# Kernel tuning notes

Measured on AMD Instinct MI355X. Metric: run time of the kernel, lower is better.

Reference implementation:

```python
import jax, jax.numpy as jnp
import numpy as np

B, M, L, HID, H, LAYERS = 16, 128, 512, 256, 4, 2
DH = HID // H  # 64 = head dim, also kernel_param dim


def _ln(x, g, b, eps=1e-5):
    mu = jnp.mean(x, axis=-1, keepdims=True)
    var = jnp.mean((x - mu) ** 2, axis=-1, keepdims=True)
    return (x - mu) / jnp.sqrt(var + eps) * g + b


def setup_inputs() -> dict:
    key = jax.random.key(0)
    ks = jax.random.split(key, 24)
    s = 0.05
    return {
        "ct_t": jax.random.uniform(ks[0], (B, M), jnp.float32),
        "ts_t": jax.random.uniform(ks[1], (B, L), jnp.float32),
        "ct_emb": jax.random.normal(ks[2], (B, M, HID), jnp.float32),
        "ts_emb": jax.random.normal(ks[3], (B, L, HID), jnp.float32),
        "kernel_param": jax.random.normal(ks[4], (DH,), jnp.float32),
        "ct_W": jax.random.normal(ks[5], (HID, HID), jnp.float32) * s,
        "ct_b": jnp.zeros((HID,), jnp.float32),
        "fW0": jax.random.normal(ks[6], (HID, HID), jnp.float32) * s,
        "fb0": jnp.zeros((HID,), jnp.float32),
        "fW1": jax.random.normal(ks[7], (HID, HID), jnp.float32) * s,
        "fb1": jnp.zeros((HID,), jnp.float32),
        "fW2": jax.random.normal(ks[8], (HID, HID), jnp.float32) * s,
        "fb2": jnp.zeros((HID,), jnp.float32),
        "f_ln_g": jnp.ones((HID,), jnp.float32),
        "f_ln_b": jnp.zeros((HID,), jnp.float32),
        "Wqkv": jax.random.normal(ks[9], (LAYERS, 3 * HID, HID), jnp.float32) * s,
        "bqkv": jnp.zeros((LAYERS, 3 * HID), jnp.float32),
        "Wo": jax.random.normal(ks[10], (LAYERS, HID, HID), jnp.float32) * s,
        "bo": jnp.zeros((LAYERS, HID), jnp.float32),
        "W1": jax.random.normal(ks[11], (LAYERS, 2 * HID, HID), jnp.float32) * s,
        "b1": jnp.zeros((LAYERS, 2 * HID), jnp.float32),
        "W2": jax.random.normal(ks[12], (LAYERS, HID, 2 * HID), jnp.float32) * s,
        "b2": jnp.zeros((LAYERS, HID), jnp.float32),
        "ln1_g": jnp.ones((LAYERS, HID), jnp.float32),
        "ln1_b": jnp.zeros((LAYERS, HID), jnp.float32),
        "ln2_g": jnp.ones((LAYERS, HID), jnp.float32),
        "ln2_b": jnp.zeros((LAYERS, HID), jnp.float32),
        "pred_W": jax.random.normal(ks[13], (1, HID), jnp.float32) * s,
        "pred_b": jnp.zeros((1,), jnp.float32),
    }


def reference(ct_t, ts_t, ct_emb, ts_emb, kernel_param, ct_W, ct_b,
              fW0, fb0, fW1, fb1, fW2, fb2, f_ln_g, f_ln_b,
              Wqkv, bqkv, Wo, bo, W1, b1, W2, b2,
              ln1_g, ln1_b, ln2_g, ln2_b, pred_W, pred_b):
    # --- TN tokenizer: multi-scale RBF kernel temporal fusion ---
    alpha = jax.nn.softplus(kernel_param)                       # [DH]  log(1+exp(p))
    ct_e = (jnp.einsum('bmd,ed->bme', ct_emb, ct_W) + ct_b)     # [B,M,HID]
    ct_e = ct_e.reshape(B, M, H, DH)
    diff = ct_t[:, :, None] - ts_t[:, None, :]                  # [B,M,L]
    norm = (diff * diff)[..., None]                             # [B,M,L,1]
    outs = []
    for s in range(H):                                          # fixed small loop over scales
        z = (-float(s)) * alpha * norm                          # [B,M,L,DH]
        w = jax.nn.logsumexp(z, axis=3, keepdims=True)          # [B,M,L,1]
        sim = jnp.exp(z - w)                                    # normalized kernel sims
        outs.append(jnp.einsum('bmnd,bmd->bnd', sim, ct_e[:, :, s, :]))  # scatter over ts events
    temp = jnp.concatenate(outs, axis=-1)                       # [B,L,HID]
    # --- Fusion module ---
    aux = jax.nn.elu(temp @ fW0.T + fb0 + ts_emb @ fW1.T + fb1)
    x = _ln(aux @ fW2.T + fb2 + ts_emb, f_ln_g, f_ln_b)         # [B,L,HID]
    # --- Transformer encoder (post-LN, gelu, no dropout at eval) ---
    inv_sqrt = 1.0 / np.sqrt(DH).astype(np.float32)
    for l in range(LAYERS):
        qkv = x @ Wqkv[l].T + bqkv[l]                           # [B,L,3*HID]
        q, k, v = jnp.split(qkv, 3, axis=-1)
        def heads(t):
            return t.reshape(B, L, H, DH).transpose(0, 2, 1, 3)
        q, k, v = heads(q), heads(k), heads(v)
        att = jax.nn.softmax(jnp.einsum('bhqd,bhkd->bhqk', q, k) * inv_sqrt, axis=-1)
        o = jnp.einsum('bhqk,bhkd->bhqd', att, v).transpose(0, 2, 1, 3).reshape(B, L, HID)
        x = _ln(x + o @ Wo[l].T + bo[l], ln1_g[l], ln1_b[l])
        ff = jax.nn.gelu(x @ W1[l].T + b1[l], approximate=False) @ W2[l].T + b2[l]
        x = _ln(x + ff, ln2_g[l], ln2_b[l])
    return x @ pred_W.T + pred_b                                # [B,L,1]
```

## Files before the change

kernel.cpp:

```cpp
#include <hip/hip_runtime.h>
#include <hip/hip_bf16.h>
#include <cstddef>

#define Bsz 16
#define Msz 128
#define Lsz 512
#define HIDs 256

typedef __attribute__((ext_vector_type(4))) float f32x4;
typedef __attribute__((ext_vector_type(8))) __bf16 bf16x8;
typedef __attribute__((ext_vector_type(8))) unsigned short ushort8;

#define CHEB_K 12
#define PI_F 3.14159265358979323846f

static __device__ inline unsigned short f2bf(float f) {
    __hip_bfloat16 h = __float2bfloat16(f);
    return *(unsigned short*)&h;
}
static __device__ inline float bf2f(unsigned short u) {
    return __builtin_bit_cast(float, (unsigned)u << 16);
}
static __device__ inline void gload16(const ushort* g, ushort* l) {
    __builtin_amdgcn_global_load_lds(
        (const __attribute__((address_space(1))) void*)g,
        (__attribute__((address_space(3))) void*)l, 16, 0, 0);
}

__global__ __launch_bounds__(256) void cheb_kernel(
    const float* __restrict__ kp, float* __restrict__ clut, float* __restrict__ cD)
{
    __shared__ float costab[CHEB_K][32];
    __shared__ float xq[32];
    __shared__ float alph[64];
    const int t = threadIdx.x;
    if (t < 64) {
        float p = kp[t];
        alph[t] = fmaxf(p, 0.f) + log1pf(__expf(-fabsf(p)));
    }
    #pragma unroll
    for (int i = 0; i < 2; i++) {
        int idx = i * 256 + t;
        if (idx < CHEB_K * 32) {
            int k = idx >> 5, q = idx & 31;
            float th = (q + 0.5f) * (PI_F / 32.f);
            costab[k][q] = __cosf((float)k * th);
        }
    }
    if (t < 32) xq[t] = 0.5f * (1.f + __cosf((t + 0.5f) * (PI_F / 32.f)));
    __syncthreads();

    if (t >= 192) return;
    const int d = t & 63, s1 = t >> 6;
    const float u = (float)(s1 + 1) * alph[d];
    float f[32];
    #pragma unroll
    for (int q = 0; q < 32; q++) f[q] = __expf(-u * xq[q]);
    #pragma unroll
    for (int k = 0; k < CHEB_K; k++) {
        float sum = 0.f;
        #pragma unroll
        for (int q = 0; q < 32; q++) sum = fmaf(f[q], costab[k][q], sum);
        float c = sum * ((k == 0 ? 1.f : 2.f) / 32.f);
        clut[s1 * (CHEB_K * 64) + k * 64 + d] = c;
        float sr = c;
        #pragma unroll
        for (int o = 1; o <= 32; o <<= 1) sr += __shfl_xor(sr, o, 64);
        if (d == 0) cD[s1 * CHEB_K + k] = sr;
    }
}

__global__ __launch_bounds__(256) void prep_kernel(
    const float* __restrict__ ts_emb, const float* __restrict__ ct_emb,
    const float* __restrict__ ct_W, const float* __restrict__ fW0,
    const float* __restrict__ fW1, const float* __restrict__ fW2,
    const float* __restrict__ Wqkv, const float* __restrict__ Wo,
    const float* __restrict__ W1, const float* __restrict__ W2,
    ushort* __restrict__ Xcat, ushort* __restrict__ Wcat,
    ushort* __restrict__ cebin, ushort* __restrict__ wct,
    ushort* __restrict__ wf2, ushort* __restrict__ wqkv,
    ushort* __restrict__ wo, ushort* __restrict__ w1, ushort* __restrict__ w2,
    const float* __restrict__ ct_t, const float* __restrict__ ts_t,
    const float* __restrict__ cD, ushort* __restrict__ invW)
{
    const int bid = blockIdx.x;
    const int tid = threadIdx.x;

    if (bid < 1920) {
        const unsigned u = bid * 256u + tid;
        const float* src; ushort* dst; unsigned rel;
        if (u < 262144u) {
            rel = u; src = ts_emb;
            dst = Xcat + ((size_t)(rel >> 5) * 512 + 256 + (rel & 31) * 8);
        } else if (u < 327680u) { rel = u - 262144u; src = ct_emb; dst = cebin + (size_t)rel * 8; }
        else if (u < 335872u) { rel = u - 327680u; src = ct_W; dst = wct + (size_t)rel * 8; }
        else if (u < 344064u) { rel = u - 335872u; src = fW0;
            dst = Wcat + ((size_t)(rel >> 5) * 512 + (rel & 31) * 8); }
        else if (u < 352256u) { rel = u - 344064u; src = fW1;
            dst = Wcat + ((size_t)(rel >> 5) * 512 + 256 + (rel & 31) * 8); }
        else if (u < 360448u) { rel = u - 352256u; src = fW2; dst = wf2 + (size_t)rel * 8; }
        else if (u < 409600u) { rel = u - 360448u; src = Wqkv; dst = wqkv + (size_t)rel * 8; }
        else if (u < 425984u) { rel = u - 409600u; src = Wo;  dst = wo + (size_t)rel * 8; }
        else if (u < 458752u) { rel = u - 425984u; src = W1;  dst = w1 + (size_t)rel * 8; }
        else                  { rel = u - 458752u; src = W2;  dst = w2 + (size_t)rel * 8; }
        float4 a = ((const float4*)src)[(size_t)rel * 2];
        float4 b = ((const float4*)src)[(size_t)rel * 2 + 1];
        ushort8 o;
        o[0] = f2bf(a.x); o[1] = f2bf(a.y); o[2] = f2bf(a.z); o[3] = f2bf(a.w);
        o[4] = f2bf(b.x); o[5] = f2bf(b.y); o[6] = f2bf(b.z); o[7] = f2bf(b.w);
        *(ushort8*)dst = o;
    } else {
        __shared__ float cd[3][CHEB_K];
        if (tid < 3 * CHEB_K) cd[tid / CHEB_K][tid % CHEB_K] = cD[tid];
        __syncthreads();

        const unsigned G = (bid - 1920) * 256u + tid;
        const int b = G >> 16;
        const int n = (G >> 7) & 511;
        const int m = G & 127;

        float x = ct_t[b * Msz + m] - ts_t[b * Lsz + n];
        x = x * x;
        const float xi = 2.f * x - 1.f;
        const float xi2 = 2.f * xi;

        float t0 = 1.f, t1 = xi;
        float a1 = cd[0][0] + cd[0][1] * xi;
        float a2 = cd[1][0] + cd[1][1] * xi;
        float a3 = cd[2][0] + cd[2][1] * xi;
        #pragma unroll
        for (int k = 2; k < CHEB_K; k++) {
            float tn = fmaf(xi2, t1, -t0);
            a1 = fmaf(cd[0][k], tn, a1);
            a2 = fmaf(cd[1][k], tn, a2);
            a3 = fmaf(cd[2][k], tn, a3);
            t0 = t1; t1 = tn;
        }
        const size_t base = ((size_t)b * 3 * Lsz + n) * Msz + m;
        invW[base]                         = f2bf(1.f / a1);
        invW[base + (size_t)Lsz * Msz]     = f2bf(1.f / a2);
        invW[base + (size_t)2 * Lsz * Msz] = f2bf(1.f / a3);
    }
}

__global__ __launch_bounds__(256) void gemm_mfma_kernel(
    const ushort* __restrict__ X, const ushort* __restrict__ W,
    const float* __restrict__ bias, const float* __restrict__ bias2,
    float* __restrict__ Yf, ushort* __restrict__ Yb,
    int NR, int K, int OUT, int act)
{
    __shared__ ushort As[2][64 * 64];
    __shared__ ushort Bs[2][128 * 64];

    const int nbx = OUT >> 7;
    const int bx = blockIdx.x % nbx;
    const int by = blockIdx.x / nbx;
    const int r0 = by << 6, o0 = bx << 7;
    const int tid = threadIdx.x;
    const int w = tid >> 6;
    const int lane = tid & 63;
    const int wr = w >> 1, wc = w & 1;
    const int lr = lane & 15, lg = lane >> 4;

    const int grow = lane >> 3;
    const int gchunk = (lane & 7) ^ grow;

    unsigned aoff[2][2], boff[4][2];
    #pragma unroll
    for (int f = 0; f < 2; f++) {
        unsigned cc = (unsigned)((lg + 4 * f) ^ (lr & 7)) * 16u;
        #pragma unroll
        for (int m = 0; m < 2; m++)
            aoff[m][f] = (unsigned)(wr * 32 + m * 16 + lr) * 128u + cc;
        #pragma unroll
        for (int n = 0; n < 4; n++)
            boff[n][f] = (unsigned)(wc * 64 + n * 16 + lr) * 128u + cc;
    }

    f32x4 acc[2][4];
    #pragma unroll
    for (int m = 0; m < 2; m++)
        #pragma unroll
        for (int n = 0; n < 4; n++) acc[m][n] = (f32x4){0.f, 0.f, 0.f, 0.f};

    const int nk = K >> 6;

    auto stage = [&](int buf, int ks) {
        const int k0 = ks << 6;
        #pragma unroll
        for (int i = 0; i < 2; i++) {
            int row = w * 16 + i * 8 + grow;
            gload16(X + (size_t)(r0 + row) * K + k0 + gchunk * 8,
                    &As[buf][(w * 16 + i * 8) * 64]);
        }
        #pragma unroll
        for (int i = 0; i < 4; i++) {
            int row = w * 32 + i * 8 + grow;
            gload16(W + (size_t)(o0 + row) * K + k0 + gchunk * 8,
                    &Bs[buf][(w * 32 + i * 8) * 64]);
        }
    };

    stage(0, 0);
    __syncthreads();
    int cur = 0;
    for (int ks = 0; ks < nk; ks++) {
        if (ks + 1 < nk) stage(cur ^ 1, ks + 1);
        const char* Ab = (const char*)As[cur];
        const char* Bb = (const char*)Bs[cur];
        #pragma unroll
        for (int f = 0; f < 2; f++) {
            bf16x8 av[2], bv[4];
            #pragma unroll
            for (int m = 0; m < 2; m++)
                av[m] = *(const bf16x8*)(Ab + aoff[m][f]);
            #pragma unroll
            for (int n = 0; n < 4; n++)
                bv[n] = *(const bf16x8*)(Bb + boff[n][f]);
            #pragma unroll
            for (int m = 0; m < 2; m++)
                #pragma unroll
                for (int n = 0; n < 4; n++)
                    acc[m][n] = __builtin_amdgcn_mfma_f32_16x16x32_bf16(
                        av[m], bv[n], acc[m][n], 0, 0, 0);
        }
        __syncthreads();
        cur ^= 1;
    }

    const int ocol0 = o0 + wc * 64;
    float bn[4];
    #pragma unroll
    for (int n = 0; n < 4; n++) {
        int o = ocol0 + n * 16 + lr;
        bn[n] = bias[o] + (bias2 ? bias2[o] : 0.f);
    }

    #pragma unroll
    for (int m = 0; m < 2; m++) {
        #pragma unroll
        for (int p = 0; p < 4; p++) {
            int r = r0 + wr * 32 + m * 16 + 4 * lg + p;
            size_t rb = (size_t)r * OUT;
            #pragma unroll
            for (int n = 0; n < 4; n++) {
                int o = ocol0 + n * 16 + lr;
                float v = acc[m][n][p] + bn[n];
                if (act == 1)      v = (v > 0.f) ? v : (__expf(v) - 1.f);
                else if (act == 2) v = 0.5f * v * (1.f + erff(v * 0.70710678118654752f));
                if (Yf) Yf[rb + o] = v;
                if (Yb) Yb[rb + o] = f2bf(v);
            }
        }
    }
}

__global__ __launch_bounds__(256) void gemm_ln_kernel(
    const ushort* __restrict__ X, const ushort* __restrict__ W,
    const float* __restrict__ bias, const float* __restrict__ add,
    const float* __restrict__ lng, const float* __restrict__ lnb,
    float* __restrict__ Xf, ushort* __restrict__ Xb,
    const float* __restrict__ predW, const float* __restrict__ predb,
    float* __restrict__ pout, int K)
{
    __shared__ ushort As[2][16 * 64];
    __shared__ ushort Bs[2][256 * 64];
    __shared__ float redA[16][4];
    __shared__ float redB[16][4];

    const int r0 = blockIdx.x << 4;
    const int tid = threadIdx.x;
    const int w = tid >> 6;
    const int lane = tid & 63;
    const int lr = lane & 15, lg = lane >> 4;
    const int grow = lane >> 3;
    const int gchunk = (lane & 7) ^ grow;

    unsigned aoff[2], boff[4][2];
    #pragma unroll
    for (int f = 0; f < 2; f++) {
        unsigned cc = (unsigned)((lg + 4 * f) ^ (lr & 7)) * 16u;
        aoff[f] = (unsigned)lr * 128u + cc;
        #pragma unroll
        for (int n = 0; n < 4; n++)
            boff[n][f] = (unsigned)(w * 64 + n * 16 + lr) * 128u + cc;
    }

    f32x4 acc[4];
    #pragma unroll
    for (int n = 0; n < 4; n++) acc[n] = (f32x4){0.f, 0.f, 0.f, 0.f};

    const int nk = K >> 6;

    auto stage = [&](int buf, int ks) {
        const int k0 = ks << 6;
        if (w < 2)
            gload16(X + (size_t)(r0 + w * 8 + grow) * K + k0 + gchunk * 8,
                    &As[buf][(w * 8) * 64]);
        #pragma unroll
        for (int i = 0; i < 8; i++) {
            gload16(W + (size_t)(w * 64 + i * 8 + grow) * K + k0 + gchunk * 8,
                    &Bs[buf][(w * 64 + i * 8) * 64]);
        }
    };

    stage(0, 0);
    __syncthreads();
    int cur = 0;
    for (int ks = 0; ks < nk; ks++) {
        if (ks + 1 < nk) stage(cur ^ 1, ks + 1);
        const char* Ab = (const char*)As[cur];
        const char* Bb = (const char*)Bs[cur];
        #pragma unroll
        for (int f = 0; f < 2; f++) {
            bf16x8 av = *(const bf16x8*)(Ab + aoff[f]);
            #pragma unroll
            for (int n = 0; n < 4; n++) {
                bf16x8 bv = *(const bf16x8*)(Bb + boff[n][f]);
                acc[n] = __builtin_amdgcn_mfma_f32_16x16x32_bf16(
                    av, bv, acc[n], 0, 0, 0);
            }
        }
        __syncthreads();
        cur ^= 1;
    }

    const int col0 = w * 64;
    float bn[4], gv[4], bv2[4], pwv[4];
    #pragma unroll
    for (int n = 0; n < 4; n++) {
        int o = col0 + n * 16 + lr;
        bn[n] = bias[o];
        gv[n] = lng[o];
        bv2[n] = lnb[o];
        pwv[n] = predW ? predW[o] : 0.f;
    }
    #pragma unroll
    for (int p = 0; p < 4; p++) {
        int r = r0 + 4 * lg + p;
        size_t rb = (size_t)r * 256;
        #pragma unroll
        for (int n = 0; n < 4; n++)
            acc[n][p] += bn[n] + add[rb + col0 + n * 16 + lr];
    }

    #pragma unroll
    for (int p = 0; p < 4; p++) {
        float s = acc[0][p] + acc[1][p] + acc[2][p] + acc[3][p];
        #pragma unroll
        for (int o = 1; o <= 8; o <<= 1) s += __shfl_xor(s, o);
        if (lr == 0) redA[4 * lg + p][w] = s;
    }
    __syncthreads();
    float mu[4];
    #pragma unroll
    for (int p = 0; p < 4; p++) {
        int row = 4 * lg + p;
        mu[p] = (redA[row][0] + redA[row][1] + redA[row][2] + redA[row][3])
                * (1.f / 256.f);
    }

    #pragma unroll
    for (int p = 0; p < 4; p++) {
        float q = 0.f;
        #pragma unroll
        for (int n = 0; n < 4; n++) {
            float dl = acc[n][p] - mu[p];
            q = fmaf(dl, dl, q);
        }
        #pragma unroll
        for (int o = 1; o <= 8; o <<= 1) q += __shfl_xor(q, o);
        if (lr == 0) redB[4 * lg + p][w] = q;
    }
    __syncthreads();

    #pragma unroll
    for (int p = 0; p < 4; p++) {
        int row = 4 * lg + p;
        float var = (redB[row][0] + redB[row][1] + redB[row][2] + redB[row][3])
                    * (1.f / 256.f);
        float rsig = rsqrtf(var + 1e-5f);
        int r = r0 + row;
        size_t rb = (size_t)r * 256;
        float pd = 0.f;
        #pragma unroll
        for (int n = 0; n < 4; n++) {
            int o = col0 + n * 16 + lr;
            float xn = (acc[n][p] - mu[p]) * rsig * gv[n] + bv2[n];
            if (Xf) Xf[rb + o] = xn;
            if (Xb) Xb[rb + o] = f2bf(xn);
            pd = fmaf(xn, pwv[n], pd);
        }
        if (predW) {
            #pragma unroll
            for (int o = 1; o <= 8; o <<= 1) pd += __shfl_xor(pd, o);
            if (lr == 0) redA[row][w] = pd;
        }
    }
    if (predW) {
        __syncthreads();
        if (tid < 16)
            pout[r0 + tid] = redA[tid][0] + redA[tid][1] + redA[tid][2]
                           + redA[tid][3] + predb[0];
    }
}

__global__ __launch_bounds__(256) void tokmix_kernel(
    const float* __restrict__ ct_t, const float* __restrict__ ts_t,
    const ushort* __restrict__ ceb, const ushort* __restrict__ invW,
    const float* __restrict__ clut, ushort* __restrict__ Xcat)
{
    const int bid = blockIdx.x;
    const int tid = threadIdx.x;

    if (bid < 384) {
        const int nt = bid & 7;
        const int s1 = (bid >> 3) % 3;
        const int b  = bid / 24;
        const int w = tid >> 6, lane = tid & 63, g = lane >> 4, r = lane & 15;

        __shared__ ushort ceT[64][136];
        __shared__ float  cl[CHEB_K][64];
        __shared__ float  cts[128];

        #pragma unroll
        for (int i = 0; i < 8; i++) {
            int idx = i * 256 + tid;
            int m = idx >> 4, d4 = (idx & 15) << 2;
            const ushort* gp = ceb + (((size_t)b * 128 + m) << 8) + (s1 + 1) * 64 + d4;
            ushort4 v = *(const ushort4*)gp;
            ceT[d4 + 0][m] = v.x; ceT[d4 + 1][m] = v.y;
            ceT[d4 + 2][m] = v.z; ceT[d4 + 3][m] = v.w;
        }
        #pragma unroll
        for (int i = 0; i < 3; i++) {
            int idx = i * 256 + tid;
            cl[idx >> 6][idx & 63] = clut[s1 * (CHEB_K * 64) + idx];
        }
        if (tid < 128) cts[tid] = ct_t[b * 128 + tid];
        __syncthreads();

        const int nrow = nt * 64 + w * 16 + r;
        const float tsn = ts_t[b * 512 + nrow];

        float xi2v[4][8], Ta[4][8], Tb[4][8];
        #pragma unroll
        for (int t4 = 0; t4 < 4; t4++) {
            int m0 = 8 * g + 32 * t4;
            ushort8 iv = *(const ushort8*)&invW[((((size_t)b * 3 + s1) * 512 + nrow) << 7) + m0];
            #pragma unroll
            for (int j = 0; j < 8; j++) {
                float dfx = cts[m0 + j] - tsn;
                float x = dfx * dfx;
                float xi = 2.f * x - 1.f;
                float w0 = bf2f(iv[j]);
                xi2v[t4][j] = 2.f * xi;
                Ta[t4][j] = w0;
                Tb[t4][j] = w0 * xi;
            }
        }

        bf16x8 cef[4][4];
        #pragma unroll
        for (int db = 0; db < 4; db++)
            #pragma unroll
            for (int t4 = 0; t4 < 4; t4++)
                cef[db][t4] = *(const bf16x8*)&ceT[db * 16 + r][8 * g + 32 * t4];

        f32x4 acc[4];
        #pragma unroll
        for (int db = 0; db < 4; db++) acc[db] = (f32x4){0.f, 0.f, 0.f, 0.f};

        #pragma unroll
        for (int k = 0; k < CHEB_K; k++) {
            if (k >= 2) {
                #pragma unroll
                for (int t4 = 0; t4 < 4; t4++)
                    #pragma unroll
                    for (int j = 0; j < 8; j++) {
                        if (k & 1) Tb[t4][j] = fmaf(xi2v[t4][j], Ta[t4][j], -Tb[t4][j]);
                        else       Ta[t4][j] = fmaf(xi2v[t4][j], Tb[t4][j], -Ta[t4][j]);
                    }
            }
            bf16x8 af[4];
            #pragma unroll
            for (int t4 = 0; t4 < 4; t4++) {
                ushort8 u;
                #pragma unroll
                for (int j = 0; j < 8; j++)
                    u[j] = f2bf((k & 1) ? Tb[t4][j] : Ta[t4][j]);
                af[t4] = __builtin_bit_cast(bf16x8, u);
            }
            #pragma unroll
            for (int db = 0; db < 4; db++) {
                f32x4 gk = (f32x4){0.f, 0.f, 0.f, 0.f};
                #pragma unroll
                for (int t4 = 0; t4 < 4; t4++)
                    gk = __builtin_amdgcn_mfma_f32_16x16x32_bf16(af[t4], cef[db][t4], gk, 0, 0, 0);
                float ck = cl[k][db * 16 + r];
                #pragma unroll
                for (int p = 0; p < 4; p++) acc[db][p] = fmaf(ck, gk[p], acc[db][p]);
            }
        }

        #pragma unroll
        for (int db = 0; db < 4; db++)
            #pragma unroll
            for (int p = 0; p < 4; p++) {
                int n_out = nt * 64 + w * 16 + 4 * g + p;
                Xcat[((size_t)b * 512 + n_out) * 512 + (s1 + 1) * 64 + db * 16 + r] =
                    f2bf(acc[db][p]);
            }
    } else {
        const int b = bid - 384;
        const int d = tid & 63, q = tid >> 6;
        float s = 0.f;
        #pragma unroll 8
        for (int i = 0; i < 32; i++) {
            int m = q * 32 + i;
            s += bf2f(ceb[(((size_t)b * 128 + m) << 8) + d]);
        }
        __shared__ float red0[4][64];
        __shared__ ushort row0[64];
        red0[q][d] = s;
        __syncthreads();
        if (tid < 64)
            row0[tid] = f2bf((red0[0][tid] + red0[1][tid] + red0[2][tid] + red0[3][tid])
                             * (1.f / 64.f));
        __syncthreads();
        #pragma unroll
        for (int i = 0; i < 16; i++) {
            int idx = i * 256 + tid;
            int n = idx >> 3, j = idx & 7;
            *(ushort8*)&Xcat[((size_t)b * 512 + n) * 512 + j * 8] =
                *(const ushort8*)&row0[j * 8];
        }
    }
}

__global__ __launch_bounds__(256) void attn_mfma_kernel(
    const ushort* __restrict__ qkv, ushort* __restrict__ Ob)
{
    const int bid = blockIdx.x;
    const int qt = bid & 7;
    const int h  = (bid >> 3) & 3;
    const int b  = bid >> 5;
    const int t  = threadIdx.x;
    const int w  = t >> 6;
    const int lane = t & 63;
    const int g = lane >> 4;
    const int r = lane & 15;

    __shared__ ushort Ks[64][72];
    __shared__ ushort Vt[64][72];
    __shared__ float  Ps[4][16][65];

    const ushort* base = qkv + (size_t)b * Lsz * 768;
    const int q0 = qt * 64 + w * 16;

    bf16x8 qf[2];
    {
        const ushort* qp = base + (size_t)(q0 + r) * 768 + h * 64 + 8 * g;
        qf[0] = __builtin_bit_cast(bf16x8, *(const ushort8*)qp);
        qf[1] = __builtin_bit_cast(bf16x8, *(const ushort8*)(qp + 32));
    }

    f32x4 Ofr[4];
    #pragma unroll
    for (int dblk = 0; dblk < 4; dblk++) Ofr[dblk] = (f32x4){0.f, 0.f, 0.f, 0.f};
    float m_run[4] = {-1e30f, -1e30f, -1e30f, -1e30f};
    float l_run[4] = {0.f, 0.f, 0.f, 0.f};

    const int srow = t >> 2;
    const int sseg = t & 3;

    ushort8 pk0, pk1, pv0, pv1;
    auto gload_chunk = [&](int c) {
        const ushort* kr = base + (size_t)(c * 64 + srow) * 768 + 256 + h * 64 + sseg * 16;
        pk0 = *(const ushort8*)kr;
        pk1 = *(const ushort8*)(kr + 8);
        pv0 = *(const ushort8*)(kr + 256);
        pv1 = *(const ushort8*)(kr + 264);
    };
    auto write_chunk = [&]() {
        *(ushort8*)&Ks[srow][sseg * 16]     = pk0;
        *(ushort8*)&Ks[srow][sseg * 16 + 8] = pk1;
        #pragma unroll
        for (int j = 0; j < 8; j++) {
            Vt[sseg * 16 + j][srow]     = pv0[j];
            Vt[sseg * 16 + 8 + j][srow] = pv1[j];
        }
    };

    gload_chunk(0);
    write_chunk();
    __syncthreads();

    for (int c = 0; c < 8; c++) {
        if (c < 7) gload_chunk(c + 1);

        f32x4 sfr[4];
        #pragma unroll
        for (int s = 0; s < 4; s++) {
            f32x4 a2 = (f32x4){0.f, 0.f, 0.f, 0.f};
            #pragma unroll
            for (int f = 0; f < 2; f++) {
                bf16x8 kf = *(const bf16x8*)&Ks[s * 16 + r][8 * g + 32 * f];
                a2 = __builtin_amdgcn_mfma_f32_16x16x32_bf16(qf[f], kf, a2, 0, 0, 0);
            }
            #pragma unroll
            for (int p = 0; p < 4; p++) a2[p] *= 0.125f;
            sfr[s] = a2;
        }

        #pragma unroll
        for (int p = 0; p < 4; p++) {
            float rm = fmaxf(fmaxf(sfr[0][p], sfr[1][p]), fmaxf(sfr[2][p], sfr[3][p]));
            #pragma unroll
            for (int o = 1; o <= 8; o <<= 1) rm = fmaxf(rm, __shfl_xor(rm, o));
            float mnew = fmaxf(m_run[p], rm);
            float sc = __expf(m_run[p] - mnew);
            m_run[p] = mnew;
            float rs = 0.f;
            #pragma unroll
            for (int s = 0; s < 4; s++) {
                float pv = __expf(sfr[s][p] - mnew);
                Ps[w][4 * g + p][s * 16 + r] = pv;
                rs += pv;
            }
            #pragma unroll
            for (int o = 1; o <= 8; o <<= 1) rs += __shfl_xor(rs, o);
            l_run[p] = l_run[p] * sc + rs;
            #pragma unroll
            for (int dblk = 0; dblk < 4; dblk++) Ofr[dblk][p] *= sc;
        }

        __asm__ volatile("s_waitcnt lgkmcnt(0)" ::: "memory");

        #pragma unroll
        for (int f = 0; f < 2; f++) {
            const float* pp = &Ps[w][r][8 * g + 32 * f];
            ushort8 ua;
            #pragma unroll
            for (int j = 0; j < 8; j++) ua[j] = f2bf(pp[j]);
            bf16x8 pa = __builtin_bit_cast(bf16x8, ua);
            #pragma unroll
            for (int dblk = 0; dblk < 4; dblk++) {
                bf16x8 vb = *(const bf16x8*)&Vt[dblk * 16 + r][32 * f + 8 * g];
                Ofr[dblk] = __builtin_amdgcn_mfma_f32_16x16x32_bf16(
                    pa, vb, Ofr[dblk], 0, 0, 0);
            }
        }

        __syncthreads();
        if (c < 7) {
            write_chunk();
            __syncthreads();
        }
    }

    #pragma unroll
    for (int dblk = 0; dblk < 4; dblk++) {
        #pragma unroll
        for (int p = 0; p < 4; p++) {
            int row = q0 + 4 * g + p;
            Ob[(size_t)(b * Lsz + row) * HIDs + h * 64 + dblk * 16 + r] =
                f2bf(Ofr[dblk][p] / l_run[p]);
        }
    }
}

extern "C" void kernel_launch(void* const* d_in, const int* in_sizes, int n_in,
                              void* d_out, int out_size, void* d_ws, size_t ws_size,
                              hipStream_t stream)
{
    (void)in_sizes; (void)n_in; (void)out_size; (void)ws_size;

    const float* ct_t   = (const float*)d_in[0];
    const float* ts_t   = (const float*)d_in[1];
    const float* ct_emb = (const float*)d_in[2];
    const float* ts_emb = (const float*)d_in[3];
    const float* kp     = (const float*)d_in[4];
    const float* ct_W   = (const float*)d_in[5];
    const float* ct_b   = (const float*)d_in[6];
    const float* fW0    = (const float*)d_in[7];
    const float* fb0    = (const float*)d_in[8];
    const float* fW1    = (const float*)d_in[9];
    const float* fb1    = (const float*)d_in[10];
    const float* fW2    = (const float*)d_in[11];
    const float* fb2    = (const float*)d_in[12];
    const float* f_ln_g = (const float*)d_in[13];
    const float* f_ln_b = (const float*)d_in[14];
    const float* Wqkv   = (const float*)d_in[15];
    const float* bqkv   = (const float*)d_in[16];
    const float* Wo     = (const float*)d_in[17];
    const float* bo     = (const float*)d_in[18];
    const float* W1     = (const float*)d_in[19];
    const float* b1     = (const float*)d_in[20];
    const float* W2     = (const float*)d_in[21];
    const float* b2     = (const float*)d_in[22];
    const float* ln1_g  = (const float*)d_in[23];
    const float* ln1_b  = (const float*)d_in[24];
    const float* ln2_g  = (const float*)d_in[25];
    const float* ln2_b  = (const float*)d_in[26];
    const float* pred_W = (const float*)d_in[27];
    const float* pred_b = (const float*)d_in[28];

    ushort* wsb = (ushort*)d_ws;
    ushort* invW  = wsb;
    ushort* auxbf = wsb;
    ushort* qkvbf = wsb;
    ushort* ff1bf = wsb;
    ushort* Xcat  = wsb + 12582912;
    ushort* Wcat  = wsb + 16777216;
    ushort* cebin = wsb + 16908288;
    ushort* cebout= wsb + 17432576;
    ushort* wct   = wsb + 17956864;
    ushort* wf2   = wsb + 18022400;
    ushort* wqkv  = wsb + 18087936;
    ushort* wo    = wsb + 18481152;
    ushort* w1    = wsb + 18612224;
    ushort* w2    = wsb + 18874368;
    ushort* xbf   = wsb + 19136512;
    ushort* obf   = wsb + 21233664;
    float*  wsf   = (float*)d_ws;
    float*  xbuf  = wsf + 11665408;
    float*  clut  = wsf + 13762560;
    float*  cDp   = wsf + 13764864;

    const int NRts = Bsz * Lsz;
    const int NRct = Bsz * Msz;
    auto grid = [](int nr, int out) { return dim3((unsigned)((nr >> 6) * (out >> 7))); };

    cheb_kernel<<<dim3(1), 256, 0, stream>>>(kp, clut, cDp);
    prep_kernel<<<dim3(1920 + 4096), 256, 0, stream>>>(
        ts_emb, ct_emb, ct_W, fW0, fW1, fW2, Wqkv, Wo, W1, W2,
        Xcat, Wcat, cebin, wct, wf2, wqkv, wo, w1, w2,
        ct_t, ts_t, cDp, invW);

    gemm_mfma_kernel<<<grid(NRct, 256), 256, 0, stream>>>(
        cebin, wct, ct_b, nullptr, nullptr, cebout, NRct, 256, 256, 0);
    tokmix_kernel<<<dim3(400), 256, 0, stream>>>(ct_t, ts_t, cebout, invW, clut, Xcat);

    gemm_mfma_kernel<<<grid(NRts, 256), 256, 0, stream>>>(
        Xcat, Wcat, fb0, fb1, nullptr, auxbf, NRts, 512, 256, 1);
    gemm_ln_kernel<<<dim3(NRts / 16), 256, 0, stream>>>(
        auxbf, wf2, fb2, ts_emb, f_ln_g, f_ln_b, xbuf, xbf,
        nullptr, nullptr, nullptr, 256);

    for (int l = 0; l < 2; l++) {
        gemm_mfma_kernel<<<grid(NRts, 768), 256, 0, stream>>>(
            xbf, wqkv + (size_t)l * 196608, bqkv + l * 768, nullptr,
            nullptr, qkvbf, NRts, 256, 768, 0);
        attn_mfma_kernel<<<dim3(512), 256, 0, stream>>>(qkvbf, obf);
        gemm_ln_kernel<<<dim3(NRts / 16), 256, 0, stream>>>(
            obf, wo + (size_t)l * 65536, bo + l * 256, xbuf,
            ln1_g + l * 256, ln1_b + l * 256, xbuf, xbf,
            nullptr, nullptr, nullptr, 256);
        gemm_mfma_kernel<<<grid(NRts, 512), 256, 0, stream>>>(
            xbf, w1 + (size_t)l * 131072, b1 + l * 512, nullptr,
            nullptr, ff1bf, NRts, 256, 512, 2);
        if (l == 0) {
            gemm_ln_kernel<<<dim3(NRts / 16), 256, 0, stream>>>(
                ff1bf, w2 + (size_t)l * 131072, b2 + l * 256, xbuf,
                ln2_g + l * 256, ln2_b + l * 256, xbuf, xbf,
                nullptr, nullptr, nullptr, 512);
        } else {
            gemm_ln_kernel<<<dim3(NRts / 16), 256, 0, stream>>>(
                ff1bf, w2 + (size_t)l * 131072, b2 + l * 256, xbuf,
                ln2_g + l * 256, ln2_b + l * 256, nullptr, nullptr,
                pred_W, pred_b, (float*)d_out, 512);
        }
    }
}
```

Baseline: 207.0 us.

## Fuse FFN GEMM pairs with LayerNorm and load GEMM operands directly from global

Each two-GEMM block (fusion aux plus fW2 projection, and the transformer W1 plus W2 FFN) now runs as one kernel. The intermediate activation stays in swizzled LDS, so the bf16 round-trip through global memory and one launch per block are removed. The plain GEMMs drop LDS staging and double buffering in favor of direct per-lane global vector loads, which relies on L2/cache reuse and may raise redundant memory traffic. The attention scale of 0.125 is folded into the Q weights and biases during prep, removing the per-score multiply.

```diff
diff --git a/kernel.cpp b/kernel.cpp
--- a/kernel.cpp
+++ b/kernel.cpp
@@ -21,10 +21,8 @@
 static __device__ inline float bf2f(unsigned short u) {
     return __builtin_bit_cast(float, (unsigned)u << 16);
 }
-static __device__ inline void gload16(const ushort* g, ushort* l) {
-    __builtin_amdgcn_global_load_lds(
-        (const __attribute__((address_space(1))) void*)g,
-        (__attribute__((address_space(3))) void*)l, 16, 0, 0);
+static __device__ inline bf16x8 ld8(const ushort* p) {
+    return __builtin_bit_cast(bf16x8, *(const ushort8*)p);
 }
 
 __global__ __launch_bounds__(256) void cheb_kernel(
@@ -81,7 +79,8 @@
     ushort* __restrict__ wf2, ushort* __restrict__ wqkv,
     ushort* __restrict__ wo, ushort* __restrict__ w1, ushort* __restrict__ w2,
     const float* __restrict__ ct_t, const float* __restrict__ ts_t,
-    const float* __restrict__ cD, ushort* __restrict__ invW)
+    const float* __restrict__ cD, ushort* __restrict__ invW,
+    const float* __restrict__ bqkv, float* __restrict__ bqs)
 {
     const int bid = blockIdx.x;
     const int tid = threadIdx.x;
@@ -89,6 +88,7 @@
     if (bid < 1920) {
         const unsigned u = bid * 256u + tid;
         const float* src; ushort* dst; unsigned rel;
+        float sc = 1.f;
         if (u < 262144u) {
             rel = u; src = ts_emb;
             dst = Xcat + ((size_t)(rel >> 5) * 512 + 256 + (rel & 31) * 8);
@@ -99,17 +99,18 @@
         else if (u < 352256u) { rel = u - 344064u; src = fW1;
             dst = Wcat + ((size_t)(rel >> 5) * 512 + 256 + (rel & 31) * 8); }
         else if (u < 360448u) { rel = u - 352256u; src = fW2; dst = wf2 + (size_t)rel * 8; }
-        else if (u < 409600u) { rel = u - 360448u; src = Wqkv; dst = wqkv + (size_t)rel * 8; }
+        else if (u < 409600u) { rel = u - 360448u; src = Wqkv; dst = wqkv + (size_t)rel * 8;
+            if (((rel >> 5) % 768) < 256) sc = 0.125f; }
         else if (u < 425984u) { rel = u - 409600u; src = Wo;  dst = wo + (size_t)rel * 8; }
         else if (u < 458752u) { rel = u - 425984u; src = W1;  dst = w1 + (size_t)rel * 8; }
         else                  { rel = u - 458752u; src = W2;  dst = w2 + (size_t)rel * 8; }
         float4 a = ((const float4*)src)[(size_t)rel * 2];
         float4 b = ((const float4*)src)[(size_t)rel * 2 + 1];
         ushort8 o;
-        o[0] = f2bf(a.x); o[1] = f2bf(a.y); o[2] = f2bf(a.z); o[3] = f2bf(a.w);
-        o[4] = f2bf(b.x); o[5] = f2bf(b.y); o[6] = f2bf(b.z); o[7] = f2bf(b.w);
+        o[0] = f2bf(a.x * sc); o[1] = f2bf(a.y * sc); o[2] = f2bf(a.z * sc); o[3] = f2bf(a.w * sc);
+        o[4] = f2bf(b.x * sc); o[5] = f2bf(b.y * sc); o[6] = f2bf(b.z * sc); o[7] = f2bf(b.w * sc);
         *(ushort8*)dst = o;
-    } else {
+    } else if (bid < 6016) {
         __shared__ float cd[3][CHEB_K];
         if (tid < 3 * CHEB_K) cd[tid / CHEB_K][tid % CHEB_K] = cD[tid];
         __syncthreads();
@@ -140,18 +141,20 @@
         invW[base]                         = f2bf(1.f / a1);
         invW[base + (size_t)Lsz * Msz]     = f2bf(1.f / a2);
         invW[base + (size_t)2 * Lsz * Msz] = f2bf(1.f / a3);
-    }
-}
-
-__global__ __launch_bounds__(256) void gemm_mfma_kernel(
+    } else {
+        #pragma unroll
+        for (int i = 0; i < 6; i++) {
+            int idx = i * 256 + tid;
+            int c = idx % 768;
+            bqs[idx] = bqkv[idx] * ((c < 256) ? 0.125f : 1.f);
+        }
+    }
+}
+
+__global__ __launch_bounds__(256) void gemm_rd_kernel(
     const ushort* __restrict__ X, const ushort* __restrict__ W,
-    const float* __restrict__ bias, const float* __restrict__ bias2,
-    float* __restrict__ Yf, ushort* __restrict__ Yb,
-    int NR, int K, int OUT, int act)
+    const float* __restrict__ bias, ushort* __restrict__ Yb, int OUT)
 {
-    __shared__ ushort As[2][64 * 64];
-    __shared__ ushort Bs[2][128 * 64];
-
     const int nbx = OUT >> 7;
     const int bx = blockIdx.x % nbx;
     const int by = blockIdx.x / nbx;
@@ -162,109 +165,67 @@
     const int wr = w >> 1, wc = w & 1;
     const int lr = lane & 15, lg = lane >> 4;
 
-    const int grow = lane >> 3;
-    const int gchunk = (lane & 7) ^ grow;
-
-    unsigned aoff[2][2], boff[4][2];
-    #pragma unroll
-    for (int f = 0; f < 2; f++) {
-        unsigned cc = (unsigned)((lg + 4 * f) ^ (lr & 7)) * 16u;
+    f32x4 acc[2][4];
+    #pragma unroll
+    for (int m = 0; m < 2; m++)
+        #pragma unroll
+        for (int n = 0; n < 4; n++) acc[m][n] = (f32x4){0.f, 0.f, 0.f, 0.f};
+
+    const ushort* ap[2];
+    const ushort* bp[4];
+    #pragma unroll
+    for (int m = 0; m < 2; m++)
+        ap[m] = X + (size_t)(r0 + wr * 32 + m * 16 + lr) * 256 + 8 * lg;
+    #pragma unroll
+    for (int n = 0; n < 4; n++)
+        bp[n] = W + (size_t)(o0 + wc * 64 + n * 16 + lr) * 256 + 8 * lg;
+
+    #pragma unroll
+    for (int ks = 0; ks < 4; ks++) {
+        bf16x8 av[2][2], bv[4][2];
         #pragma unroll
         for (int m = 0; m < 2; m++)
-            aoff[m][f] = (unsigned)(wr * 32 + m * 16 + lr) * 128u + cc;
+            #pragma unroll
+            for (int f = 0; f < 2; f++)
+                av[m][f] = ld8(ap[m] + ks * 64 + 32 * f);
         #pragma unroll
         for (int n = 0; n < 4; n++)
-            boff[n][f] = (unsigned)(wc * 64 + n * 16 + lr) * 128u + cc;
-    }
-
-    f32x4 acc[2][4];
-    #pragma unroll
-    for (int m = 0; m < 2; m++)
-        #pragma unroll
-        for (int n = 0; n < 4; n++) acc[m][n] = (f32x4){0.f, 0.f, 0.f, 0.f};
-
-    const int nk = K >> 6;
-
-    auto stage = [&](int buf, int ks) {
-        const int k0 = ks << 6;
-        #pragma unroll
-        for (int i = 0; i < 2; i++) {
-            int row = w * 16 + i * 8 + grow;
-            gload16(X + (size_t)(r0 + row) * K + k0 + gchunk * 8,
-                    &As[buf][(w * 16 + i * 8) * 64]);
-        }
-        #pragma unroll
-        for (int i = 0; i < 4; i++) {
-            int row = w * 32 + i * 8 + grow;
-            gload16(W + (size_t)(o0 + row) * K + k0 + gchunk * 8,
-                    &Bs[buf][(w * 32 + i * 8) * 64]);
-        }
-    };
-
-    stage(0, 0);
-    __syncthreads();
-    int cur = 0;
-    for (int ks = 0; ks < nk; ks++) {
-        if (ks + 1 < nk) stage(cur ^ 1, ks + 1);
-        const char* Ab = (const char*)As[cur];
-        const char* Bb = (const char*)Bs[cur];
-        #pragma unroll
-        for (int f = 0; f < 2; f++) {
-            bf16x8 av[2], bv[4];
-            #pragma unroll
-            for (int m = 0; m < 2; m++)
-                av[m] = *(const bf16x8*)(Ab + aoff[m][f]);
-            #pragma unroll
-            for (int n = 0; n < 4; n++)
-                bv[n] = *(const bf16x8*)(Bb + boff[n][f]);
+            #pragma unroll
+            for (int f = 0; f < 2; f++)
+                bv[n][f] = ld8(bp[n] + ks * 64 + 32 * f);
+        #pragma unroll
+        for (int f = 0; f < 2; f++)
             #pragma unroll
             for (int m = 0; m < 2; m++)
                 #pragma unroll
                 for (int n = 0; n < 4; n++)
                     acc[m][n] = __builtin_amdgcn_mfma_f32_16x16x32_bf16(
-                        av[m], bv[n], acc[m][n], 0, 0, 0);
-        }
-        __syncthreads();
-        cur ^= 1;
+                        av[m][f], bv[n][f], acc[m][n], 0, 0, 0);
     }
 
     const int ocol0 = o0 + wc * 64;
     float bn[4];
     #pragma unroll
-    for (int n = 0; n < 4; n++) {
-        int o = ocol0 + n * 16 + lr;
-        bn[n] = bias[o] + (bias2 ? bias2[o] : 0.f);
-    }
-
-    #pragma unroll
-    for (int m = 0; m < 2; m++) {
+    for (int n = 0; n < 4; n++) bn[n] = bias[ocol0 + n * 16 + lr];
+
+    #pragma unroll
+    for (int m = 0; m < 2; m++)
         #pragma unroll
         for (int p = 0; p < 4; p++) {
             int r = r0 + wr * 32 + m * 16 + 4 * lg + p;
             size_t rb = (size_t)r * OUT;
             #pragma unroll
-            for (int n = 0; n < 4; n++) {
-                int o = ocol0 + n * 16 + lr;
-                float v = acc[m][n][p] + bn[n];
-                if (act == 1)      v = (v > 0.f) ? v : (__expf(v) - 1.f);
-                else if (act == 2) v = 0.5f * v * (1.f + erff(v * 0.70710678118654752f));
-                if (Yf) Yf[rb + o] = v;
-                if (Yb) Yb[rb + o] = f2bf(v);
-            }
-        }
-    }
-}
-
-__global__ __launch_bounds__(256) void gemm_ln_kernel(
+            for (int n = 0; n < 4; n++)
+                Yb[rb + ocol0 + n * 16 + lr] = f2bf(acc[m][n][p] + bn[n]);
+        }
+}
+
+__global__ __launch_bounds__(256) void gemm_ln_rd_kernel(
     const ushort* __restrict__ X, const ushort* __restrict__ W,
     const float* __restrict__ bias, const float* __restrict__ add,
     const float* __restrict__ lng, const float* __restrict__ lnb,
-    float* __restrict__ Xf, ushort* __restrict__ Xb,
-    const float* __restrict__ predW, const float* __restrict__ predb,
-    float* __restrict__ pout, int K)
+    float* __restrict__ Xf, ushort* __restrict__ Xb)
 {
-    __shared__ ushort As[2][16 * 64];
-    __shared__ ushort Bs[2][256 * 64];
     __shared__ float redA[16][4];
     __shared__ float redB[16][4];
 
@@ -273,72 +234,40 @@
     const int w = tid >> 6;
     const int lane = tid & 63;
     const int lr = lane & 15, lg = lane >> 4;
-    const int grow = lane >> 3;
-    const int gchunk = (lane & 7) ^ grow;
-
-    unsigned aoff[2], boff[4][2];
-    #pragma unroll
-    for (int f = 0; f < 2; f++) {
-        unsigned cc = (unsigned)((lg + 4 * f) ^ (lr & 7)) * 16u;
-        aoff[f] = (unsigned)lr * 128u + cc;
+    const int col0 = w * 64;
+
+    f32x4 acc[4];
+    #pragma unroll
+    for (int n = 0; n < 4; n++) acc[n] = (f32x4){0.f, 0.f, 0.f, 0.f};
+
+    const ushort* ap = X + (size_t)(r0 + lr) * 256 + 8 * lg;
+    const ushort* bp[4];
+    #pragma unroll
+    for (int n = 0; n < 4; n++)
+        bp[n] = W + (size_t)(col0 + n * 16 + lr) * 256 + 8 * lg;
+
+    #pragma unroll
+    for (int ks = 0; ks < 4; ks++) {
+        bf16x8 av[2];
+        #pragma unroll
+        for (int f = 0; f < 2; f++) av[f] = ld8(ap + ks * 64 + 32 * f);
         #pragma unroll
         for (int n = 0; n < 4; n++)
-            boff[n][f] = (unsigned)(w * 64 + n * 16 + lr) * 128u + cc;
-    }
-
-    f32x4 acc[4];
-    #pragma unroll
-    for (int n = 0; n < 4; n++) acc[n] = (f32x4){0.f, 0.f, 0.f, 0.f};
-
-    const int nk = K >> 6;
-
-    auto stage = [&](int buf, int ks) {
-        const int k0 = ks << 6;
-        if (w < 2)
-            gload16(X + (size_t)(r0 + w * 8 + grow) * K + k0 + gchunk * 8,
-                    &As[buf][(w * 8) * 64]);
-        #pragma unroll
-        for (int i = 0; i < 8; i++) {
-            gload16(W + (size_t)(w * 64 + i * 8 + grow) * K + k0 + gchunk * 8,
-                    &Bs[buf][(w * 64 + i * 8) * 64]);
-        }
-    };
-
-    stage(0, 0);
-    __syncthreads();
-    int cur = 0;
-    for (int ks = 0; ks < nk; ks++) {
-        if (ks + 1 < nk) stage(cur ^ 1, ks + 1);
-        const char* Ab = (const char*)As[cur];
-        const char* Bb = (const char*)Bs[cur];
-        #pragma unroll
-        for (int f = 0; f < 2; f++) {
-            bf16x8 av = *(const bf16x8*)(Ab + aoff[f]);
-            #pragma unroll
-            for (int n = 0; n < 4; n++) {
-                bf16x8 bv = *(const bf16x8*)(Bb + boff[n][f]);
+            #pragma unroll
+            for (int f = 0; f < 2; f++)
                 acc[n] = __builtin_amdgcn_mfma_f32_16x16x32_bf16(
-                    av, bv, acc[n], 0, 0, 0);
-            }
-        }
-        __syncthreads();
-        cur ^= 1;
-    }
-
-    const int col0 = w * 64;
-    float bn[4], gv[4], bv2[4], pwv[4];
+                    av[f], ld8(bp[n] + ks * 64 + 32 * f), acc[n], 0, 0, 0);
+    }
+
+    float bn[4], gv[4], bv2[4];
     #pragma unroll
     for (int n = 0; n < 4; n++) {
         int o = col0 + n * 16 + lr;
-        bn[n] = bias[o];
-        gv[n] = lng[o];
-        bv2[n] = lnb[o];
-        pwv[n] = predW ? predW[o] : 0.f;
-    }
-    #pragma unroll
-    for (int p = 0; p < 4; p++) {
-        int r = r0 + 4 * lg + p;
-        size_t rb = (size_t)r * 256;
+        bn[n] = bias[o]; gv[n] = lng[o]; bv2[n] = lnb[o];
+    }
+    #pragma unroll
+    for (int p = 0; p < 4; p++) {
+        size_t rb = (size_t)(r0 + 4 * lg + p) * 256;
         #pragma unroll
         for (int n = 0; n < 4; n++)
             acc[n][p] += bn[n] + add[rb + col0 + n * 16 + lr];
@@ -356,10 +285,8 @@
     #pragma unroll
     for (int p = 0; p < 4; p++) {
         int row = 4 * lg + p;
-        mu[p] = (redA[row][0] + redA[row][1] + redA[row][2] + redA[row][3])
-                * (1.f / 256.f);
-    }
-
+        mu[p] = (redA[row][0] + redA[row][1] + redA[row][2] + redA[row][3]) * (1.f / 256.f);
+    }
     #pragma unroll
     for (int p = 0; p < 4; p++) {
         float q = 0.f;
@@ -373,20 +300,156 @@
         if (lr == 0) redB[4 * lg + p][w] = q;
     }
     __syncthreads();
-
     #pragma unroll
     for (int p = 0; p < 4; p++) {
         int row = 4 * lg + p;
-        float var = (redB[row][0] + redB[row][1] + redB[row][2] + redB[row][3])
-                    * (1.f / 256.f);
+        float var = (redB[row][0] + redB[row][1] + redB[row][2] + redB[row][3]) * (1.f / 256.f);
         float rsig = rsqrtf(var + 1e-5f);
-        int r = r0 + row;
-        size_t rb = (size_t)r * 256;
-        float pd = 0.f;
+        size_t rb = (size_t)(r0 + row) * 256;
         #pragma unroll
         for (int n = 0; n < 4; n++) {
             int o = col0 + n * 16 + lr;
             float xn = (acc[n][p] - mu[p]) * rsig * gv[n] + bv2[n];
+            Xf[rb + o] = xn;
+            Xb[rb + o] = f2bf(xn);
+        }
+    }
+}
+
+template<int K1, int MID, int ACT>
+__global__ __launch_bounds__(256) void ffn_fused_kernel(
+    const ushort* __restrict__ X, const ushort* __restrict__ W1m,
+    const float* __restrict__ b1v, const float* __restrict__ b1b,
+    const ushort* __restrict__ W2m, const float* __restrict__ b2v,
+    const float* __restrict__ add,
+    const float* __restrict__ lng, const float* __restrict__ lnb,
+    float* __restrict__ Xf, ushort* __restrict__ Xb,
+    const float* __restrict__ predW, const float* __restrict__ predb,
+    float* __restrict__ pout)
+{
+    constexpr int NS = MID / 64;
+    constexpr int SL = MID / 4;
+    __shared__ ushort Gs[16][MID + 8];
+    __shared__ float redA[16][4];
+    __shared__ float redB[16][4];
+
+    const int r0 = blockIdx.x << 4;
+    const int tid = threadIdx.x;
+    const int w = tid >> 6;
+    const int lane = tid & 63;
+    const int lr = lane & 15, lg = lane >> 4;
+
+    f32x4 acc1[NS];
+    #pragma unroll
+    for (int n = 0; n < NS; n++) acc1[n] = (f32x4){0.f, 0.f, 0.f, 0.f};
+
+    const ushort* ap = X + (size_t)(r0 + lr) * K1 + 8 * lg;
+    #pragma unroll
+    for (int ks = 0; ks < K1 / 64; ks++) {
+        bf16x8 av[2];
+        #pragma unroll
+        for (int f = 0; f < 2; f++) av[f] = ld8(ap + ks * 64 + 32 * f);
+        #pragma unroll
+        for (int n = 0; n < NS; n++) {
+            const ushort* bp = W1m + (size_t)(w * SL + n * 16 + lr) * K1 + ks * 64 + 8 * lg;
+            #pragma unroll
+            for (int f = 0; f < 2; f++)
+                acc1[n] = __builtin_amdgcn_mfma_f32_16x16x32_bf16(
+                    av[f], ld8(bp + 32 * f), acc1[n], 0, 0, 0);
+        }
+    }
+    #pragma unroll
+    for (int n = 0; n < NS; n++) {
+        int col = w * SL + n * 16 + lr;
+        float bb = b1v[col] + (b1b ? b1b[col] : 0.f);
+        #pragma unroll
+        for (int p = 0; p < 4; p++) {
+            float v = acc1[n][p] + bb;
+            if (ACT == 1) v = (v > 0.f) ? v : (__expf(v) - 1.f);
+            else          v = 0.5f * v * (1.f + erff(v * 0.70710678118654752f));
+            int row = 4 * lg + p;
+            int ch = (col >> 3) ^ (row & 7);
+            Gs[row][ch * 8 + (col & 7)] = f2bf(v);
+        }
+    }
+    __syncthreads();
+
+    const int col0 = w * 64;
+    f32x4 acc2[4];
+    #pragma unroll
+    for (int n = 0; n < 4; n++) acc2[n] = (f32x4){0.f, 0.f, 0.f, 0.f};
+
+    #pragma unroll
+    for (int ks = 0; ks < MID / 64; ks++) {
+        bf16x8 av[2];
+        #pragma unroll
+        for (int f = 0; f < 2; f++) {
+            int ch = (ks * 8 + lg + 4 * f) ^ (lr & 7);
+            av[f] = ld8(&Gs[lr][ch * 8]);
+        }
+        #pragma unroll
+        for (int n = 0; n < 4; n++) {
+            const ushort* bp = W2m + (size_t)(col0 + n * 16 + lr) * MID + ks * 64 + 8 * lg;
+            #pragma unroll
+            for (int f = 0; f < 2; f++)
+                acc2[n] = __builtin_amdgcn_mfma_f32_16x16x32_bf16(
+                    av[f], ld8(bp + 32 * f), acc2[n], 0, 0, 0);
+        }
+    }
+
+    float bn[4], gv[4], bv2[4], pwv[4];
+    #pragma unroll
+    for (int n = 0; n < 4; n++) {
+        int o = col0 + n * 16 + lr;
+        bn[n] = b2v[o]; gv[n] = lng[o]; bv2[n] = lnb[o];
+        pwv[n] = predW ? predW[o] : 0.f;
+    }
+    #pragma unroll
+    for (int p = 0; p < 4; p++) {
+        size_t rb = (size_t)(r0 + 4 * lg + p) * 256;
+        #pragma unroll
+        for (int n = 0; n < 4; n++)
+            acc2[n][p] += bn[n] + add[rb + col0 + n * 16 + lr];
+    }
+
+    #pragma unroll
+    for (int p = 0; p < 4; p++) {
+        float s = acc2[0][p] + acc2[1][p] + acc2[2][p] + acc2[3][p];
+        #pragma unroll
+        for (int o = 1; o <= 8; o <<= 1) s += __shfl_xor(s, o);
+        if (lr == 0) redA[4 * lg + p][w] = s;
+    }
+    __syncthreads();
+    float mu[4];
+    #pragma unroll
+    for (int p = 0; p < 4; p++) {
+        int row = 4 * lg + p;
+        mu[p] = (redA[row][0] + redA[row][1] + redA[row][2] + redA[row][3]) * (1.f / 256.f);
+    }
+    #pragma unroll
+    for (int p = 0; p < 4; p++) {
+        float q = 0.f;
+        #pragma unroll
+        for (int n = 0; n < 4; n++) {
+            float dl = acc2[n][p] - mu[p];
+            q = fmaf(dl, dl, q);
+        }
+        #pragma unroll
+        for (int o = 1; o <= 8; o <<= 1) q += __shfl_xor(q, o);
+        if (lr == 0) redB[4 * lg + p][w] = q;
+    }
+    __syncthreads();
+    #pragma unroll
+    for (int p = 0; p < 4; p++) {
+        int row = 4 * lg + p;
+        float var = (redB[row][0] + redB[row][1] + redB[row][2] + redB[row][3]) * (1.f / 256.f);
+        float rsig = rsqrtf(var + 1e-5f);
+        size_t rb = (size_t)(r0 + row) * 256;
+        float pd = 0.f;
+        #pragma unroll
+        for (int n = 0; n < 4; n++) {
+            int o = col0 + n * 16 + lr;
+            float xn = (acc2[n][p] - mu[p]) * rsig * gv[n] + bv2[n];
             if (Xf) Xf[rb + o] = xn;
             if (Xb) Xb[rb + o] = f2bf(xn);
             pd = fmaf(xn, pwv[n], pd);
@@ -561,8 +624,8 @@
     bf16x8 qf[2];
     {
         const ushort* qp = base + (size_t)(q0 + r) * 768 + h * 64 + 8 * g;
-        qf[0] = __builtin_bit_cast(bf16x8, *(const ushort8*)qp);
-        qf[1] = __builtin_bit_cast(bf16x8, *(const ushort8*)(qp + 32));
+        qf[0] = ld8(qp);
+        qf[1] = ld8(qp + 32);
     }
 
     f32x4 Ofr[4];
@@ -608,8 +671,6 @@
                 bf16x8 kf = *(const bf16x8*)&Ks[s * 16 + r][8 * g + 32 * f];
                 a2 = __builtin_amdgcn_mfma_f32_16x16x32_bf16(qf[f], kf, a2, 0, 0, 0);
             }
-            #pragma unroll
-            for (int p = 0; p < 4; p++) a2[p] *= 0.125f;
             sfr[s] = a2;
         }
 
@@ -708,9 +769,7 @@
 
     ushort* wsb = (ushort*)d_ws;
     ushort* invW  = wsb;
-    ushort* auxbf = wsb;
     ushort* qkvbf = wsb;
-    ushort* ff1bf = wsb;
     ushort* Xcat  = wsb + 12582912;
     ushort* Wcat  = wsb + 16777216;
     ushort* cebin = wsb + 16908288;
@@ -727,49 +786,41 @@
     float*  xbuf  = wsf + 11665408;
     float*  clut  = wsf + 13762560;
     float*  cDp   = wsf + 13764864;
+    float*  bqs   = wsf + 13764928;
 
     const int NRts = Bsz * Lsz;
     const int NRct = Bsz * Msz;
     auto grid = [](int nr, int out) { return dim3((unsigned)((nr >> 6) * (out >> 7))); };
 
     cheb_kernel<<<dim3(1), 256, 0, stream>>>(kp, clut, cDp);
-    prep_kernel<<<dim3(1920 + 4096), 256, 0, stream>>>(
+    prep_kernel<<<dim3(1920 + 4096 + 1), 256, 0, stream>>>(
         ts_emb, ct_emb, ct_W, fW0, fW1, fW2, Wqkv, Wo, W1, W2,
         Xcat, Wcat, cebin, wct, wf2, wqkv, wo, w1, w2,
-        ct_t, ts_t, cDp, invW);
-
-    gemm_mfma_kernel<<<grid(NRct, 256), 256, 0, stream>>>(
-        cebin, wct, ct_b, nullptr, nullptr, cebout, NRct, 256, 256, 0);
+        ct_t, ts_t, cDp, invW, bqkv, bqs);
+
+    gemm_rd_kernel<<<grid(NRct, 256), 256, 0, stream>>>(cebin, wct, ct_b, cebout, 256);
     tokmix_kernel<<<dim3(400), 256, 0, stream>>>(ct_t, ts_t, cebout, invW, clut, Xcat);
 
-    gemm_mfma_kernel<<<grid(NRts, 256), 256, 0, stream>>>(
-        Xcat, Wcat, fb0, fb1, nullptr, auxbf, NRts, 512, 256, 1);
-    gemm_ln_kernel<<<dim3(NRts / 16), 256, 0, stream>>>(
-        auxbf, wf2, fb2, ts_emb, f_ln_g, f_ln_b, xbuf, xbf,
-        nullptr, nullptr, nullptr, 256);
+    ffn_fused_kernel<512, 256, 1><<<dim3(NRts / 16), 256, 0, stream>>>(
+        Xcat, Wcat, fb0, fb1, wf2, fb2, ts_emb, f_ln_g, f_ln_b,
+        xbuf, xbf, nullptr, nullptr, nullptr);
 
     for (int l = 0; l < 2; l++) {
-        gemm_mfma_kernel<<<grid(NRts, 768), 256, 0, stream>>>(
-            xbf, wqkv + (size_t)l * 196608, bqkv + l * 768, nullptr,
-            nullptr, qkvbf, NRts, 256, 768, 0);
+        gemm_rd_kernel<<<grid(NRts, 768), 256, 0, stream>>>(
+            xbf, wqkv + (size_t)l * 196608, bqs + l * 768, qkvbf, 768);
         attn_mfma_kernel<<<dim3(512), 256, 0, stream>>>(qkvbf, obf);
-        gemm_ln_kernel<<<dim3(NRts / 16), 256, 0, stream>>>(
+        gemm_ln_rd_kernel<<<dim3(NRts / 16), 256, 0, stream>>>(
             obf, wo + (size_t)l * 65536, bo + l * 256, xbuf,
-            ln1_g + l * 256, ln1_b + l * 256, xbuf, xbf,
-            nullptr, nullptr, nullptr, 256);
-        gemm_mfma_kernel<<<grid(NRts, 512), 256, 0, stream>>>(
-            xbf, w1 + (size_t)l * 131072, b1 + l * 512, nullptr,
-            nullptr, ff1bf, NRts, 256, 512, 2);
+            ln1_g + l * 256, ln1_b + l * 256, xbuf, xbf);
         if (l == 0) {
-            gemm_ln_kernel<<<dim3(NRts / 16), 256, 0, stream>>>(
-                ff1bf, w2 + (size_t)l * 131072, b2 + l * 256, xbuf,
-                ln2_g + l * 256, ln2_b + l * 256, xbuf, xbf,
-                nullptr, nullptr, nullptr, 512);
+            ffn_fused_kernel<256, 512, 2><<<dim3(NRts / 16), 256, 0, stream>>>(
+                xbf, w1, b1, nullptr, w2, b2, xbuf,
+                ln2_g, ln2_b, xbuf, xbf, nullptr, nullptr, nullptr);
         } else {
-            gemm_ln_kernel<<<dim3(NRts / 16), 256, 0, stream>>>(
-                ff1bf, w2 + (size_t)l * 131072, b2 + l * 256, xbuf,
-                ln2_g + l * 256, ln2_b + l * 256, nullptr, nullptr,
-                pred_W, pred_b, (float*)d_out, 512);
-        }
-    }
-}
+            ffn_fused_kernel<256, 512, 2><<<dim3(NRts / 16), 256, 0, stream>>>(
+                xbf, w1 + 131072, b1 + 512, nullptr, w2 + 131072, b2 + 256, xbuf,
+                ln2_g + 256, ln2_b + 256, nullptr, nullptr,
+                pred_W, pred_b, (float*)d_out);
+        }
+    }
+}
```

After: 268.7 us. +29.8%, slower.
